# Kernel optimization log

Hardware: AMD Instinct MI355X
Metric: run time of the kernel (lower is better)

Reference implementation:

```python
import jax, jax.numpy as jnp
import numpy as np

B, S, I, H = 64, 2048, 256, 256


def setup_inputs() -> dict:
    key = jax.random.key(0)
    ks = jax.random.split(key, 13)
    s_i = 1.0 / np.sqrt(I)
    s_h = 1.0 / np.sqrt(H)
    inp = {
        "input_seq": jax.random.normal(ks[0], (B, S, I), dtype=jnp.float32),
        "Wz": jax.random.uniform(ks[1], (I, H), jnp.float32, -s_i, s_i),
        "bz": jax.random.uniform(ks[2], (H,), jnp.float32, -s_i, s_i),
        "Wr": jax.random.uniform(ks[3], (I, H), jnp.float32, -s_i, s_i),
        "br": jax.random.uniform(ks[4], (H,), jnp.float32, -s_i, s_i),
        "Wh": jax.random.uniform(ks[5], (I, H), jnp.float32, -s_i, s_i),
        "bh": jax.random.uniform(ks[6], (H,), jnp.float32, -s_i, s_i),
        "Uz": jax.random.uniform(ks[7], (H, H), jnp.float32, -s_h, s_h),
        "buz": jax.random.uniform(ks[8], (H,), jnp.float32, -s_h, s_h),
        "Ur": jax.random.uniform(ks[9], (H, H), jnp.float32, -s_h, s_h),
        "bur": jax.random.uniform(ks[10], (H,), jnp.float32, -s_h, s_h),
        "Uh": jax.random.uniform(ks[11], (H, H), jnp.float32, -s_h, s_h),
        "buh": jax.random.uniform(ks[12], (H,), jnp.float32, -s_h, s_h),
    }
    return inp


def reference(input_seq, Wz, bz, Wr, br, Wh, bh, Uz, buz, Ur, bur, Uh, buh):
    # Precompute all input-side GEMMs in one batched pass: [B,S,H] each
    xz = jnp.einsum("bsi,ih->bsh", input_seq, Wz) + bz
    xr = jnp.einsum("bsi,ih->bsh", input_seq, Wr) + br
    xh = jnp.einsum("bsi,ih->bsh", input_seq, Wh) + bh
    # Time-major for scan: [S,B,H]
    xs = (xz.transpose(1, 0, 2), xr.transpose(1, 0, 2), xh.transpose(1, 0, 2))

    def step(h_prev, x_t):
        xz_t, xr_t, xh_t = x_t
        z = jax.nn.sigmoid(xz_t + h_prev @ Uz + buz)
        r = jax.nn.sigmoid(xr_t + h_prev @ Ur + bur)
        cand = jnp.tanh(xh_t + r * (h_prev @ Uh + buh))
        h_t = (1.0 - z) * h_prev + z * cand
        return h_t, h_t

    h0 = jnp.zeros((input_seq.shape[0], Uz.shape[0]), dtype=input_seq.dtype)
    _, hs = jax.lax.scan(step, h0, xs)  # hs: [S,B,H]
    return hs.transpose(1, 0, 2)  # [B,S,H]
```

## Files before the change

### kernel.cpp

```cpp
#include <hip/hip_runtime.h>
#include <hip/hip_bf16.h>
#include <hip/hip_fp16.h>


#define S_LEN 2048
#define BATCH 64
#define HDIM  256
#define NGATE 768
#define M_TOTAL (BATCH * S_LEN)

typedef _Float16 h8_t __attribute__((ext_vector_type(8)));
typedef float    f32x4 __attribute__((ext_vector_type(4)));
typedef int      i32x4 __attribute__((ext_vector_type(4)));

static __device__ __forceinline__ float h2f(unsigned short s) {
    _Float16 h; __builtin_memcpy(&h, &s, 2); return (float)h;
}
static __device__ __forceinline__ unsigned short f2h(float f) {
    _Float16 h = (_Float16)f; unsigned short s; __builtin_memcpy(&s, &h, 2); return s;
}

static __device__ __forceinline__ float sigmoid_fast(float x) {
    float e = __builtin_amdgcn_exp2f(-1.44269504088896341f * x);
    return __builtin_amdgcn_rcpf(1.0f + e);
}
static __device__ __forceinline__ float tanh_fast(float x) {
    return 2.0f * sigmoid_fast(2.0f * x) - 1.0f;
}


__global__ void k_cvt_x(const float4* __restrict__ x4, ushort4* __restrict__ xh4) {
    int i = blockIdx.x * blockDim.x + threadIdx.x;
    float4 v = x4[i];
    ushort4 o;
    o.x = f2h(v.x); o.y = f2h(v.y); o.z = f2h(v.z); o.w = f2h(v.w);
    xh4[i] = o;
}

__global__ void k_prep_w(const float* __restrict__ Wz, const float* __restrict__ Wr,
                         const float* __restrict__ Wh,
                         const float* __restrict__ bz, const float* __restrict__ br,
                         const float* __restrict__ bh,
                         const float* __restrict__ buz, const float* __restrict__ bur,
                         unsigned short* __restrict__ Wt, float* __restrict__ biascat) {
    int n = blockIdx.x;
    int k = threadIdx.x;
    int g = n >> 8, h = n & 255;
    const float* W = (g == 0) ? Wz : (g == 1) ? Wr : Wh;
    Wt[n * 256 + k] = f2h(W[k * 256 + h]);
    if (k == 0) {
        float bias = (g == 0) ? (bz[h] + buz[h]) : (g == 1) ? (br[h] + bur[h]) : bh[h];
        biascat[n] = bias;
    }
}

__global__ void k_prep_uq(const float* __restrict__ Uz, const float* __restrict__ Ur,
                          const float* __restrict__ Uh,
                          signed char* __restrict__ Ufrag, float* __restrict__ invU) {
    int blk = blockIdx.x;
    int g = blk >> 8, col = blk & 255;
    int k = threadIdx.x;
    const float* U = (g == 0) ? Uz : (g == 1) ? Ur : Uh;
    float v = U[k * 256 + col];
    __shared__ float red[256];
    red[k] = fabsf(v);
    __syncthreads();
    for (int off = 128; off > 0; off >>= 1) {
        if (k < off) red[k] = fmaxf(red[k], red[k + off]);
        __syncthreads();
    }
    float m = red[0];
    float s = (m > 0.0f) ? 127.0f / m : 0.0f;
    int q = __float2int_rn(v * s);
    q = max(-127, min(127, q));
    int ks = k >> 6, l4 = (k >> 4) & 3, e = k & 15;
    int l = l4 * 16 + (col & 15), nt = col >> 4;
    Ufrag[((size_t)(((g * 16 + nt) * 4 + ks) * 64 + l)) * 16 + e] = (signed char)q;
    if (k == 0) invU[g * 256 + col] = m * (1.0f / 16129.0f);
}


#define LDT 264

__global__ __launch_bounds__(256) void k_gemm_x(const unsigned short* __restrict__ Xh,
                                                const unsigned short* __restrict__ Wt,
                                                const float* __restrict__ biascat,
                                                unsigned short* __restrict__ XG) {
    __shared__ unsigned short As[128 * LDT];
    __shared__ unsigned short Bs[128 * LDT];
    int tid = threadIdx.x;
    int m0 = blockIdx.x * 128;
    int n0 = blockIdx.y * 128;

    {
        const unsigned short* ga = Xh + (size_t)m0 * 256;
        const unsigned short* gb = Wt + (size_t)n0 * 256;
#pragma unroll
        for (int i = 0; i < 16; i++) {
            int chunk = tid + i * 256;
            int row = chunk >> 5;
            int c8  = (chunk & 31) * 8;
            uint4 va = *(const uint4*)(ga + row * 256 + c8);
            *(uint4*)(As + row * LDT + c8) = va;
            uint4 vb = *(const uint4*)(gb + row * 256 + c8);
            *(uint4*)(Bs + row * LDT + c8) = vb;
        }
    }
    __syncthreads();

    int lane = tid & 63, wv = tid >> 6;
    int mw = (wv & 1) * 64, nw = (wv >> 1) * 64;
    int lr = lane & 15, lg = lane >> 4;

    f32x4 acc[4][4] = {};
#pragma unroll
    for (int k = 0; k < 8; k++) {
        h8_t a[4], b[4];
#pragma unroll
        for (int i = 0; i < 4; i++)
            a[i] = *(const h8_t*)(As + (mw + i * 16 + lr) * LDT + k * 32 + lg * 8);
#pragma unroll
        for (int jj = 0; jj < 4; jj++)
            b[jj] = *(const h8_t*)(Bs + (nw + jj * 16 + lr) * LDT + k * 32 + lg * 8);
#pragma unroll
        for (int i = 0; i < 4; i++)
#pragma unroll
            for (int jj = 0; jj < 4; jj++)
                acc[i][jj] = __builtin_amdgcn_mfma_f32_16x16x32_f16(a[i], b[jj], acc[i][jj], 0, 0, 0);
    }

#pragma unroll
    for (int jj = 0; jj < 4; jj++) {
        int gcol = n0 + nw + jj * 16 + lr;
        float bias = biascat[gcol];
#pragma unroll
        for (int i = 0; i < 4; i++) {
            int grow = m0 + mw + i * 16 + lg * 4;
#pragma unroll
            for (int r = 0; r < 4; r++) {
                XG[(size_t)(grow + r) * NGATE + gcol] = f2h(acc[i][jj][r] + bias);
            }
        }
    }
}


__global__ __launch_bounds__(256) __attribute__((amdgpu_waves_per_eu(1, 1)))
void k_gru(const i32x4* __restrict__ Ufrag,
           const float* __restrict__ invU,
           const unsigned short* __restrict__ XG,
           const float* __restrict__ buh,
           float* __restrict__ out) {
    __shared__ __align__(16) signed char hb[2][256];
    int tid = threadIdx.x;
    int lane = tid & 63, w = tid >> 6;
    int l4 = lane >> 4, lc = lane & 15;
    int b = blockIdx.x;
    int c = (w * 4 + l4) * 16 + lc;

    i32x4 uf[3][4][4];
#pragma unroll
    for (int g = 0; g < 3; g++)
#pragma unroll
        for (int i = 0; i < 4; i++)
#pragma unroll
            for (int ks = 0; ks < 4; ks++)
                uf[g][i][ks] = Ufrag[(size_t)((g * 16 + (w * 4 + i)) * 4 + ks) * 64 + lane];
#pragma unroll
    for (int g = 0; g < 3; g++)
#pragma unroll
        for (int i = 0; i < 4; i++)
#pragma unroll
            for (int ks = 0; ks < 4; ks++)
                asm volatile("" : "+v"(uf[g][i][ks]));

    float invz = invU[0 * 256 + c], invr = invU[1 * 256 + c], invh = invU[2 * 256 + c];
    float buh_c = buh[c];

    if (tid < 64) ((int*)hb[0])[tid] = 0;

    const unsigned short* xb = XG + (size_t)b * S_LEN * NGATE;
    float* ob = out + (size_t)b * S_LEN * HDIM;

    const unsigned short* xp = xb + c;
    unsigned short pz = xp[0], pr = xp[256], ph = xp[512];
    xp += NGATE;
    float hm = 0.0f;
    bool s0 = (l4 & 1) != 0, s1 = (l4 & 2) != 0;
    __syncthreads();

    for (int t = 0; t < S_LEN; ++t) {
        const signed char* hrow = hb[t & 1];
        signed char* hdst = hb[(t & 1) ^ 1];

        i32x4 acc[3][4] = {};
#pragma unroll
        for (int ks = 0; ks < 4; ks++) {
            i32x4 a = *(const i32x4*)(hrow + ks * 64 + l4 * 16);
#pragma unroll
            for (int g = 0; g < 3; g++)
#pragma unroll
                for (int i = 0; i < 4; i++)
                    acc[g][i] = __builtin_amdgcn_mfma_i32_16x16x64_i8(a, uf[g][i][ks], acc[g][i], 0, 0, 0);
        }

        int z01 = s0 ? acc[0][1][0] : acc[0][0][0];
        int z23 = s0 ? acc[0][3][0] : acc[0][2][0];
        float vz = (float)(s1 ? z23 : z01) * invz;
        int r01 = s0 ? acc[1][1][0] : acc[1][0][0];
        int r23 = s0 ? acc[1][3][0] : acc[1][2][0];
        float vr = (float)(s1 ? r23 : r01) * invr;
        int h01 = s0 ? acc[2][1][0] : acc[2][0][0];
        int h23 = s0 ? acc[2][3][0] : acc[2][2][0];
        float vh = (float)(s1 ? h23 : h01) * invh;

        float z = sigmoid_fast(h2f(pz) + vz);
        float r = sigmoid_fast(h2f(pr) + vr);
        float cd = tanh_fast(h2f(ph) + r * (vh + buh_c));
        hm = (1.0f - z) * hm + z * cd;

        ob[(size_t)t * HDIM + c] = hm;
        hdst[c] = (signed char)__float2int_rn(hm * 127.0f);

        pz = xp[0]; pr = xp[256]; ph = xp[512];
        xp += NGATE;
        __syncthreads();
    }
}


extern "C" void kernel_launch(void* const* d_in, const int* in_sizes, int n_in,
                              void* d_out, int out_size, void* d_ws, size_t ws_size,
                              hipStream_t stream) {
    const float* x   = (const float*)d_in[0];
    const float* Wz  = (const float*)d_in[1];
    const float* bz  = (const float*)d_in[2];
    const float* Wr  = (const float*)d_in[3];
    const float* br  = (const float*)d_in[4];
    const float* Wh  = (const float*)d_in[5];
    const float* bh  = (const float*)d_in[6];
    const float* Uz  = (const float*)d_in[7];
    const float* buz = (const float*)d_in[8];
    const float* Ur  = (const float*)d_in[9];
    const float* bur = (const float*)d_in[10];
    const float* Uh  = (const float*)d_in[11];
    const float* buh = (const float*)d_in[12];

    char* ws = (char*)d_ws;
    unsigned short* Xh = (unsigned short*)(ws);
    unsigned short* XG = (unsigned short*)(ws + 67108864);
    unsigned short* Wt = (unsigned short*)(ws + 268435456);
    signed char*    Ufrag = (signed char*)(ws + 268828672);
    float*          biascat = (float*)(ws + 269221888);
    float*          invU = (float*)(ws + 269225984);

    k_cvt_x<<<32768, 256, 0, stream>>>((const float4*)x, (ushort4*)Xh);
    k_prep_w<<<768, 256, 0, stream>>>(Wz, Wr, Wh, bz, br, bh, buz, bur, Wt, biascat);
    k_prep_uq<<<768, 256, 0, stream>>>(Uz, Ur, Uh, Ufrag, invU);

    dim3 g1(M_TOTAL / 128, NGATE / 128);
    k_gemm_x<<<g1, 256, 0, stream>>>(Xh, Wt, biascat, XG);

    k_gru<<<BATCH, 256, 0, stream>>>((const i32x4*)Ufrag, invU, XG, buh, (float*)d_out);
}
```

Baseline: 1.293 ms.

## Split GRU recurrence across 8 waves with half the MFMA tiles each

The recurrent kernel now runs with 512 threads (8 waves) per batch element, and each wave owns 2 instead of 4 column tiles per gate. This halves the serial MFMA chain and register-resident U fragments per wave. Lanes in the upper half of each wave compute redundantly and only the lower half writes output and the quantized hidden state. It also starts each accumulator from a zero register and raises wave priority during the MFMA section. The cost is a larger block barrier every step and redundant elementwise work in half the lanes.

```diff
diff --git a/kernel.cpp b/kernel.cpp
--- a/kernel.cpp
+++ b/kernel.cpp
@@ -145,7 +145,7 @@
 }
 
 
-__global__ __launch_bounds__(256) __attribute__((amdgpu_waves_per_eu(1, 1)))
+__global__ __launch_bounds__(512) __attribute__((amdgpu_waves_per_eu(2, 2)))
 void k_gru(const i32x4* __restrict__ Ufrag,
            const float* __restrict__ invU,
            const unsigned short* __restrict__ XG,
@@ -156,23 +156,28 @@
     int lane = tid & 63, w = tid >> 6;
     int l4 = lane >> 4, lc = lane & 15;
     int b = blockIdx.x;
-    int c = (w * 4 + l4) * 16 + lc;
-
-    i32x4 uf[3][4][4];
+    int sel = l4 & 1;
+    int c = (2 * w + sel) * 16 + lc;
+    bool writer = (l4 < 2);
+
+    i32x4 uf[3][2][4];
 #pragma unroll
     for (int g = 0; g < 3; g++)
 #pragma unroll
-        for (int i = 0; i < 4; i++)
+        for (int i = 0; i < 2; i++)
 #pragma unroll
             for (int ks = 0; ks < 4; ks++)
-                uf[g][i][ks] = Ufrag[(size_t)((g * 16 + (w * 4 + i)) * 4 + ks) * 64 + lane];
+                uf[g][i][ks] = Ufrag[(size_t)((g * 16 + (2 * w + i)) * 4 + ks) * 64 + lane];
 #pragma unroll
     for (int g = 0; g < 3; g++)
 #pragma unroll
-        for (int i = 0; i < 4; i++)
+        for (int i = 0; i < 2; i++)
 #pragma unroll
             for (int ks = 0; ks < 4; ks++)
                 asm volatile("" : "+v"(uf[g][i][ks]));
+
+    i32x4 zc = {};
+    asm volatile("" : "+v"(zc));
 
     float invz = invU[0 * 256 + c], invr = invU[1 * 256 + c], invh = invU[2 * 256 + c];
     float buh_c = buh[c];
@@ -186,41 +191,46 @@
     unsigned short pz = xp[0], pr = xp[256], ph = xp[512];
     xp += NGATE;
     float hm = 0.0f;
-    bool s0 = (l4 & 1) != 0, s1 = (l4 & 2) != 0;
     __syncthreads();
 
     for (int t = 0; t < S_LEN; ++t) {
         const signed char* hrow = hb[t & 1];
         signed char* hdst = hb[(t & 1) ^ 1];
 
-        i32x4 acc[3][4] = {};
-#pragma unroll
-        for (int ks = 0; ks < 4; ks++) {
+        i32x4 acc[3][2];
+        __builtin_amdgcn_s_setprio(1);
+        {
+            i32x4 a = *(const i32x4*)(hrow + l4 * 16);
+#pragma unroll
+            for (int g = 0; g < 3; g++)
+#pragma unroll
+                for (int i = 0; i < 2; i++)
+                    acc[g][i] = __builtin_amdgcn_mfma_i32_16x16x64_i8(a, uf[g][i][0], zc, 0, 0, 0);
+        }
+#pragma unroll
+        for (int ks = 1; ks < 4; ks++) {
             i32x4 a = *(const i32x4*)(hrow + ks * 64 + l4 * 16);
 #pragma unroll
             for (int g = 0; g < 3; g++)
 #pragma unroll
-                for (int i = 0; i < 4; i++)
+                for (int i = 0; i < 2; i++)
                     acc[g][i] = __builtin_amdgcn_mfma_i32_16x16x64_i8(a, uf[g][i][ks], acc[g][i], 0, 0, 0);
         }
-
-        int z01 = s0 ? acc[0][1][0] : acc[0][0][0];
-        int z23 = s0 ? acc[0][3][0] : acc[0][2][0];
-        float vz = (float)(s1 ? z23 : z01) * invz;
-        int r01 = s0 ? acc[1][1][0] : acc[1][0][0];
-        int r23 = s0 ? acc[1][3][0] : acc[1][2][0];
-        float vr = (float)(s1 ? r23 : r01) * invr;
-        int h01 = s0 ? acc[2][1][0] : acc[2][0][0];
-        int h23 = s0 ? acc[2][3][0] : acc[2][2][0];
-        float vh = (float)(s1 ? h23 : h01) * invh;
+        __builtin_amdgcn_s_setprio(0);
+
+        float vz = (float)(sel ? acc[0][1][0] : acc[0][0][0]) * invz;
+        float vr = (float)(sel ? acc[1][1][0] : acc[1][0][0]) * invr;
+        float vh = (float)(sel ? acc[2][1][0] : acc[2][0][0]) * invh;
 
         float z = sigmoid_fast(h2f(pz) + vz);
         float r = sigmoid_fast(h2f(pr) + vr);
         float cd = tanh_fast(h2f(ph) + r * (vh + buh_c));
         hm = (1.0f - z) * hm + z * cd;
 
-        ob[(size_t)t * HDIM + c] = hm;
-        hdst[c] = (signed char)__float2int_rn(hm * 127.0f);
+        if (writer) {
+            ob[(size_t)t * HDIM + c] = hm;
+            hdst[c] = (signed char)__float2int_rn(hm * 127.0f);
+        }
 
         pz = xp[0]; pr = xp[256]; ph = xp[512];
         xp += NGATE;
@@ -261,5 +271,5 @@
     dim3 g1(M_TOTAL / 128, NGATE / 128);
     k_gemm_x<<<g1, 256, 0, stream>>>(Xh, Wt, biascat, XG);
 
-    k_gru<<<BATCH, 256, 0, stream>>>((const i32x4*)Ufrag, invU, XG, buh, (float*)d_out);
-}
+    k_gru<<<BATCH, 512, 0, stream>>>((const i32x4*)Ufrag, invU, XG, buh, (float*)d_out);
+}
```

Result: no change. 1.282 ms (-0.9%).
